# Performance work log

Hardware: AMD Instinct MI355X
Metric: run time of the kernel (lower is better)

## Reference

```python
import jax, jax.numpy as jnp
import numpy as np
from jax import lax

B, S = 32, 128
E, H, V = 300, 1024, 32000


def setup_inputs() -> dict:
    key = jax.random.key(0)
    ks = jax.random.split(key, 6)
    scale = 0.02
    return {
        "sent": jax.random.randint(ks[0], (B, S), 0, V),
        "length": jax.random.randint(ks[1], (B,), 0, S - 1),
        "wordvec": jax.random.normal(ks[2], (V, E), dtype=jnp.float32) * scale,
        "Wxh": jax.random.normal(ks[3], (E, H), dtype=jnp.float32) * scale,
        "Whh": jax.random.normal(ks[4], (H, H), dtype=jnp.float32) * scale,
        "bh": jnp.zeros((H,), dtype=jnp.float32),
        "Wout": jax.random.normal(ks[5], (H, V), dtype=jnp.float32) * scale,
        "bout": jnp.zeros((V,), dtype=jnp.float32),
    }


def reference(sent, length, wordvec, Wxh, Whh, bh, Wout, bout):
    # Embedding lookup for all input positions except the last (teacher forcing)
    emb = wordvec[sent]                      # [B, S, E]
    xs = jnp.swapaxes(emb[:, :-1], 0, 1)     # [S-1, B, E] time-major for scan

    def step(h, x):
        # vanilla RNN cell: h' = tanh(x Wxh + h Whh + b)
        h_new = jnp.tanh(x @ Wxh + h @ Whh + bh)
        return h_new, h_new

    h0 = jnp.zeros((sent.shape[0], Whh.shape[0]), dtype=wordvec.dtype)
    _, hs = lax.scan(step, h0, xs)           # hs: [S-1, B, H]

    # Per-step vocab projection, batched across time in one GEMM
    logits = jnp.einsum('sbh,hv->bsv', hs, Wout) + bout   # [B, S-1, V]

    # Masked cross-entropy against next tokens
    targets = sent[:, 1:]                                  # [B, S-1]
    logp = jax.nn.log_softmax(logits, axis=-1)
    nll = -jnp.take_along_axis(logp, targets[..., None], axis=-1)[..., 0]
    seqlen = sent.shape[1]
    valid = (jnp.arange(seqlen - 1)[None, :] < length[:, None]).astype(logits.dtype)
    loss = (nll * valid).sum() / valid.sum()
    return loss, logits
```

## Files before the change

### kernel.cpp

```cpp
#include <hip/hip_runtime.h>
#include <hip/hip_bf16.h>
#include <stdint.h>

#define B_ 32
#define S_ 128
#define SM1 127
#define E_ 300
#define H_ 1024
#define V_ 32000
#define M_ 4064

typedef __bf16 bf16x8 __attribute__((ext_vector_type(8)));
typedef float f32x4 __attribute__((ext_vector_type(4)));

#define WS_CTR   0
#define WS_NLL   1024
#define WS_HFRAG 4096
#define WS_PRE   135168
#define WS_HS    16781312
#define WS_WBT   25104384

union frag_cvt { f32x4 f; bf16x8 h; };

__device__ __forceinline__ f32x4 coh_load16(const uint8_t* p) {
  f32x4 r;
  asm volatile("global_load_dwordx4 %0, %1, off sc0 sc1"
               : "=v"(r) : "v"(p) : "memory");
  return r;
}
__device__ __forceinline__ void coh_store16(uint8_t* p, f32x4 v) {
  asm volatile("global_store_dwordx4 %0, %1, off sc0 sc1"
               :: "v"(p), "v"(v) : "memory");
}

__global__ __launch_bounds__(256) void k_wout_cvt(const float* __restrict__ Wout,
                                                  __hip_bfloat16* __restrict__ bt) {
  __shared__ float t[32][33];
  int vt = blockIdx.x / 32, kt = blockIdx.x - vt * 32;
  int tx = threadIdx.x & 31, ty = threadIdx.x >> 5;
#pragma unroll
  for (int i = 0; i < 4; i++) {
    int k = kt * 32 + ty + i * 8;
    t[ty + i * 8][tx] = Wout[(size_t)k * V_ + vt * 32 + tx];
  }
  __syncthreads();
#pragma unroll
  for (int i = 0; i < 4; i++) {
    int v = vt * 32 + ty + i * 8;
    bt[(size_t)v * H_ + kt * 32 + tx] = __float2bfloat16(t[tx][ty + i * 8]);
  }
}

__global__ __launch_bounds__(256) void k_pre(const int* __restrict__ sent,
    const float* __restrict__ wordvec, const float* __restrict__ Wxh,
    const float* __restrict__ bh, float* __restrict__ pre) {
  __shared__ float e[8 * E_];
  int r0 = blockIdx.x * 8;
  int s = r0 >> 5, b0 = r0 & 31;
  for (int idx = threadIdx.x; idx < 8 * E_; idx += 256) {
    int i = idx / E_, k = idx - i * E_;
    int tok = sent[(b0 + i) * S_ + s];
    e[idx] = wordvec[(size_t)tok * E_ + k];
  }
  __syncthreads();
  int j0 = threadIdx.x * 4;
  float4 acc[8];
#pragma unroll
  for (int i = 0; i < 8; i++) acc[i] = make_float4(0.f, 0.f, 0.f, 0.f);
  for (int k = 0; k < E_; k++) {
    float4 w = *(const float4*)&Wxh[k * H_ + j0];
#pragma unroll
    for (int i = 0; i < 8; i++) {
      float ev = e[i * E_ + k];
      acc[i].x += ev * w.x; acc[i].y += ev * w.y;
      acc[i].z += ev * w.z; acc[i].w += ev * w.w;
    }
  }
  float4 bias = *(const float4*)&bh[j0];
#pragma unroll
  for (int i = 0; i < 8; i++) {
    float4 o = make_float4(acc[i].x + bias.x, acc[i].y + bias.y,
                           acc[i].z + bias.z, acc[i].w + bias.w);
    *(float4*)&pre[(size_t)(r0 + i) * H_ + j0] = o;
  }
}

__global__ __launch_bounds__(256) void k_rnn(const float* __restrict__ Whh,
    const float* __restrict__ pre, __hip_bfloat16* __restrict__ hs,
    uint8_t* __restrict__ ws) {
  __shared__ __hip_bfloat16 ldsB[32 * 64 * 8];
  __shared__ float ldsP[4 * 8 * 64];
  __shared__ __hip_bfloat16 ldsCt[32 * 24];
  const int jb = blockIdx.x;
  const int tid = threadIdx.x;
  const int lane = tid & 63, w = tid >> 6;
  uint32_t* ctr = (uint32_t*)(ws + WS_CTR);
  uint8_t* hfrag = ws + WS_HFRAG;

  for (int idx = tid; idx < 32 * 64; idx += 256) {
    int kc = idx >> 6, l = idx & 63;
    int n = l & 15;
    int k0 = kc * 32 + ((l >> 4) << 3);
    bf16x8 v;
#pragma unroll
    for (int i = 0; i < 8; i++)
      v[i] = (__bf16)Whh[(size_t)(k0 + i) * H_ + jb * 16 + n];
    *(bf16x8*)&ldsB[idx * 8] = v;
  }
  __syncthreads();

  for (int s = 0; s < SM1; s++) {
    const uint8_t* rbuf = hfrag + ((s & 1) ? 65536 : 0);
    uint8_t* wbuf = hfrag + ((s & 1) ? 0 : 65536);
    f32x4 acc0 = {0.f, 0.f, 0.f, 0.f}, acc1 = {0.f, 0.f, 0.f, 0.f};
    const int kc0 = w * 8;

    bf16x8 a0[8], a1[8];
#pragma unroll
    for (int i = 0; i < 8; i++) {
      int kc = kc0 + i;
      frag_cvt c0, c1;
      c0.f = coh_load16(rbuf + (((kc * 2 + 0) * 64 + lane) << 4));
      c1.f = coh_load16(rbuf + (((kc * 2 + 1) * 64 + lane) << 4));
      a0[i] = c0.h; a1[i] = c1.h;
    }
    asm volatile("s_waitcnt vmcnt(0)" ::: "memory");
    __builtin_amdgcn_sched_barrier(0);
#pragma unroll
    for (int i = 0; i < 8; i++) {
      int kc = kc0 + i;
      bf16x8 b0 = *(const bf16x8*)&ldsB[(kc * 64 + lane) * 8];
      acc0 = __builtin_amdgcn_mfma_f32_16x16x32_bf16(a0[i], b0, acc0, 0, 0, 0);
      acc1 = __builtin_amdgcn_mfma_f32_16x16x32_bf16(a1[i], b0, acc1, 0, 0, 0);
    }
#pragma unroll
    for (int r = 0; r < 4; r++) {
      ldsP[(w * 8 + r) * 64 + lane] = acc0[r];
      ldsP[(w * 8 + 4 + r) * 64 + lane] = acc1[r];
    }
    __syncthreads();
    {
      int t = w >> 1;
      int jl = lane & 15;
#pragma unroll
      for (int rr = 0; rr < 2; rr++) {
        int r = ((w & 1) << 1) + rr;
        float sum = 0.f;
#pragma unroll
        for (int p = 0; p < 4; p++) sum += ldsP[(p * 8 + t * 4 + r) * 64 + lane];
        int b = t * 16 + ((lane >> 4) << 2) + r;
        float x = sum + pre[(size_t)(s * 32 + b) * H_ + jb * 16 + jl];
        float h = tanhf(x);
        __hip_bfloat16 hb = __float2bfloat16(h);
        hs[(size_t)(b * SM1 + s) * H_ + jb * 16 + jl] = hb;
        ldsCt[b * 24 + jl] = hb;
      }
    }
    __syncthreads();
    if (w == 0 && (lane >> 5) == (jb & 1)) {
      int kcw = jb >> 1;
#pragma unroll
      for (int t2 = 0; t2 < 2; t2++) {
        frag_cvt c;
        c.h = *(const bf16x8*)&ldsCt[(t2 * 16 + (lane & 15)) * 24 +
                                     (((lane >> 4) & 1) << 3)];
        coh_store16(wbuf + (((kcw * 2 + t2) * 64 + lane) << 4), c.f);
      }
    }
    if (s < SM1 - 1) {
      if (tid == 0) {
        asm volatile("s_waitcnt vmcnt(0)" ::: "memory");
        __hip_atomic_fetch_add(&ctr[s], 1u, __ATOMIC_RELAXED, __HIP_MEMORY_SCOPE_AGENT);
        while (__hip_atomic_load(&ctr[s], __ATOMIC_RELAXED, __HIP_MEMORY_SCOPE_AGENT) < 64u)
          __builtin_amdgcn_s_sleep(2);
      }
      __syncthreads();
    }
  }
}

__global__ __launch_bounds__(256) void k_gemm(const __hip_bfloat16* __restrict__ A,
    const __hip_bfloat16* __restrict__ Bt, const float* __restrict__ bout,
    float* __restrict__ C) {
  __shared__ __hip_bfloat16 lA[128 * 64];
  __shared__ __hip_bfloat16 lB[128 * 64];
  int bid = blockIdx.x;
  int idx = bid & 255;
  int mt = idx & 31;
  int nt = ((bid >> 8) << 3) + (idx >> 5);
  int tid = threadIdx.x;
  int lane = tid & 63, w = tid >> 6;
  int wm = (w >> 1) << 6, wn = (w & 1) << 6;
  int mbase = mt * 128, nbase = nt * 128;
  f32x4 acc[4][4];
#pragma unroll
  for (int t = 0; t < 4; t++)
#pragma unroll
    for (int u = 0; u < 4; u++) acc[t][u] = (f32x4){0.f, 0.f, 0.f, 0.f};

  for (int k0 = 0; k0 < H_; k0 += 64) {
#pragma unroll
    for (int r = 0; r < 4; r++) {
      int L = r * 4096 + tid * 16;
      int row = L >> 7;
      int gphys = (L >> 4) & 7;
      int glog = gphys ^ (row & 7);
      int m = mbase + row; if (m > M_ - 1) m = M_ - 1;
      const uint8_t* g = (const uint8_t*)A + ((size_t)m * H_ + k0) * 2 + glog * 16;
      __builtin_amdgcn_global_load_lds((const __attribute__((address_space(1))) uint32_t*)g,
          (__attribute__((address_space(3))) uint32_t*)((uint8_t*)lA + L), 16, 0, 0);
    }
#pragma unroll
    for (int r = 0; r < 4; r++) {
      int L = r * 4096 + tid * 16;
      int row = L >> 7;
      int gphys = (L >> 4) & 7;
      int glog = gphys ^ (row & 7);
      int n = nbase + row;
      const uint8_t* g = (const uint8_t*)Bt + ((size_t)n * H_ + k0) * 2 + glog * 16;
      __builtin_amdgcn_global_load_lds((const __attribute__((address_space(1))) uint32_t*)g,
          (__attribute__((address_space(3))) uint32_t*)((uint8_t*)lB + L), 16, 0, 0);
    }
    __builtin_amdgcn_s_waitcnt(0);
    __syncthreads();
#pragma unroll
    for (int kk = 0; kk < 64; kk += 32) {
      bf16x8 af[4], bfr[4];
      int quad = lane >> 4;
#pragma unroll
      for (int t = 0; t < 4; t++) {
        int row = wm + t * 16 + (lane & 15);
        int gphys = ((kk >> 3) + quad) ^ (row & 7);
        af[t] = *(const bf16x8*)&lA[row * 64 + gphys * 8];
      }
#pragma unroll
      for (int u = 0; u < 4; u++) {
        int row = wn + u * 16 + (lane & 15);
        int gphys = ((kk >> 3) + quad) ^ (row & 7);
        bfr[u] = *(const bf16x8*)&lB[row * 64 + gphys * 8];
      }
#pragma unroll
      for (int t = 0; t < 4; t++)
#pragma unroll
        for (int u = 0; u < 4; u++)
          acc[t][u] = __builtin_amdgcn_mfma_f32_16x16x32_bf16(af[t], bfr[u], acc[t][u], 0, 0, 0);
    }
    __syncthreads();
  }
  int quad = lane >> 4, l15 = lane & 15;
#pragma unroll
  for (int u = 0; u < 4; u++) {
    int col = nbase + wn + u * 16 + l15;
    float bias = bout[col];
#pragma unroll
    for (int t = 0; t < 4; t++) {
      int rowb = mbase + wm + t * 16 + quad * 4;
#pragma unroll
      for (int r = 0; r < 4; r++) {
        int row = rowb + r;
        if (row < M_) C[(size_t)row * V_ + col] = acc[t][u][r] + bias;
      }
    }
  }
}

__global__ __launch_bounds__(256) void k_loss(const float* __restrict__ logits,
    const int* __restrict__ sent, const int* __restrict__ length,
    float* __restrict__ nll_acc) {
  int r = blockIdx.x;
  int b = r / SM1, s = r - b * SM1;
  if (s >= length[b]) return;
  const float* row = logits + (size_t)r * V_;
  float m = -3.0e38f, l = 0.f;
  for (int v = threadIdx.x; v < V_; v += 256) {
    float x = row[v];
    float nm = fmaxf(m, x);
    l = l * __expf(m - nm) + __expf(x - nm);
    m = nm;
  }
#pragma unroll
  for (int off = 1; off < 64; off <<= 1) {
    float m2 = __shfl_xor(m, off);
    float l2 = __shfl_xor(l, off);
    float nm = fmaxf(m, m2);
    l = l * __expf(m - nm) + l2 * __expf(m2 - nm);
    m = nm;
  }
  __shared__ float sm[4], sl[4];
  int wv = threadIdx.x >> 6;
  if ((threadIdx.x & 63) == 0) { sm[wv] = m; sl[wv] = l; }
  __syncthreads();
  if (threadIdx.x == 0) {
    m = sm[0]; l = sl[0];
    for (int p = 1; p < 4; p++) {
      float nm = fmaxf(m, sm[p]);
      l = l * __expf(m - nm) + sl[p] * __expf(sm[p] - nm);
      m = nm;
    }
    int tgt = sent[b * S_ + s + 1];
    float nll = m + logf(l) - row[tgt];
    atomicAdd(nll_acc, nll);
  }
}

__global__ void k_final(const float* __restrict__ nll_acc,
                        const int* __restrict__ length, float* __restrict__ out) {
  float cnt = 0.f;
  for (int b = 0; b < B_; b++) cnt += (float)length[b];
  out[0] = nll_acc[0] / cnt;
}

extern "C" void kernel_launch(void* const* d_in, const int* in_sizes, int n_in,
                              void* d_out, int out_size, void* d_ws, size_t ws_size,
                              hipStream_t stream) {
  const int* sent      = (const int*)d_in[0];
  const int* length    = (const int*)d_in[1];
  const float* wordvec = (const float*)d_in[2];
  const float* Wxh     = (const float*)d_in[3];
  const float* Whh     = (const float*)d_in[4];
  const float* bh      = (const float*)d_in[5];
  const float* Wout    = (const float*)d_in[6];
  const float* bout    = (const float*)d_in[7];
  float* out = (float*)d_out;
  uint8_t* ws = (uint8_t*)d_ws;

  hipMemsetAsync(ws, 0, 135168, stream);

  __hip_bfloat16* wbt = (__hip_bfloat16*)(ws + WS_WBT);
  float* pre          = (float*)(ws + WS_PRE);
  __hip_bfloat16* hs  = (__hip_bfloat16*)(ws + WS_HS);
  float* logits       = out + 1;

  k_wout_cvt<<<32000, 256, 0, stream>>>(Wout, wbt);
  k_pre<<<508, 256, 0, stream>>>(sent, wordvec, Wxh, bh, pre);
  k_rnn<<<64, 256, 0, stream>>>(Whh, pre, hs, ws);
  k_gemm<<<8000, 256, 0, stream>>>(hs, wbt, bout, logits);
  k_loss<<<4064, 256, 0, stream>>>(logits, sent, length, (float*)(ws + WS_NLL));
  k_final<<<1, 1, 0, stream>>>((const float*)(ws + WS_NLL), length, out);
}
```

Before: 1.959 ms.

## Double-buffer LDS tiles in vocab GEMM and stage epilogue through LDS

The vocab-projection GEMM now keeps two LDS buffers and issues the global-to-LDS loads for the next K-slice before running MFMAs on the current one, which overlaps memory latency with compute. The epilogue writes accumulators into a padded per-wave LDS tile and then stores rows to global memory as 16-byte vectors instead of scattered scalar stores. In exchange, LDS use grows to about 68 KB per block, which can lower occupancy.

```diff
diff --git a/kernel.cpp b/kernel.cpp
--- a/kernel.cpp
+++ b/kernel.cpp
@@ -182,8 +182,7 @@
 __global__ __launch_bounds__(256) void k_gemm(const __hip_bfloat16* __restrict__ A,
     const __hip_bfloat16* __restrict__ Bt, const float* __restrict__ bout,
     float* __restrict__ C) {
-  __shared__ __hip_bfloat16 lA[128 * 64];
-  __shared__ __hip_bfloat16 lB[128 * 64];
+  __shared__ __align__(16) uint8_t lds[69632];
   int bid = blockIdx.x;
   int idx = bid & 255;
   int mt = idx & 31;
@@ -192,74 +191,92 @@
   int lane = tid & 63, w = tid >> 6;
   int wm = (w >> 1) << 6, wn = (w & 1) << 6;
   int mbase = mt * 128, nbase = nt * 128;
+  int quad = lane >> 4, l15 = lane & 15;
   f32x4 acc[4][4];
 #pragma unroll
   for (int t = 0; t < 4; t++)
 #pragma unroll
     for (int u = 0; u < 4; u++) acc[t][u] = (f32x4){0.f, 0.f, 0.f, 0.f};
 
-  for (int k0 = 0; k0 < H_; k0 += 64) {
+  auto STAGE = [&](int buf, int k0) {
+    uint8_t* dA = lds + buf * 32768;
+    uint8_t* dB = lds + buf * 32768 + 16384;
 #pragma unroll
     for (int r = 0; r < 4; r++) {
       int L = r * 4096 + tid * 16;
       int row = L >> 7;
-      int gphys = (L >> 4) & 7;
-      int glog = gphys ^ (row & 7);
+      int glog = ((L >> 4) & 7) ^ (row & 7);
       int m = mbase + row; if (m > M_ - 1) m = M_ - 1;
       const uint8_t* g = (const uint8_t*)A + ((size_t)m * H_ + k0) * 2 + glog * 16;
       __builtin_amdgcn_global_load_lds((const __attribute__((address_space(1))) uint32_t*)g,
-          (__attribute__((address_space(3))) uint32_t*)((uint8_t*)lA + L), 16, 0, 0);
+          (__attribute__((address_space(3))) uint32_t*)(dA + L), 16, 0, 0);
     }
 #pragma unroll
     for (int r = 0; r < 4; r++) {
       int L = r * 4096 + tid * 16;
       int row = L >> 7;
-      int gphys = (L >> 4) & 7;
-      int glog = gphys ^ (row & 7);
+      int glog = ((L >> 4) & 7) ^ (row & 7);
       int n = nbase + row;
       const uint8_t* g = (const uint8_t*)Bt + ((size_t)n * H_ + k0) * 2 + glog * 16;
       __builtin_amdgcn_global_load_lds((const __attribute__((address_space(1))) uint32_t*)g,
-          (__attribute__((address_space(3))) uint32_t*)((uint8_t*)lB + L), 16, 0, 0);
-    }
-    __builtin_amdgcn_s_waitcnt(0);
-    __syncthreads();
+          (__attribute__((address_space(3))) uint32_t*)(dB + L), 16, 0, 0);
+    }
+  };
+
+  STAGE(0, 0);
+  asm volatile("s_waitcnt vmcnt(0)" ::: "memory");
+  __syncthreads();
+
+  for (int t = 0; t < 16; t++) {
+    int cur = t & 1;
+    if (t < 15) STAGE(cur ^ 1, (t + 1) * 64);
+    const __hip_bfloat16* lA = (const __hip_bfloat16*)(lds + cur * 32768);
+    const __hip_bfloat16* lB = (const __hip_bfloat16*)(lds + cur * 32768 + 16384);
 #pragma unroll
     for (int kk = 0; kk < 64; kk += 32) {
       bf16x8 af[4], bfr[4];
-      int quad = lane >> 4;
-#pragma unroll
-      for (int t = 0; t < 4; t++) {
-        int row = wm + t * 16 + (lane & 15);
+#pragma unroll
+      for (int tt = 0; tt < 4; tt++) {
+        int row = wm + tt * 16 + l15;
         int gphys = ((kk >> 3) + quad) ^ (row & 7);
-        af[t] = *(const bf16x8*)&lA[row * 64 + gphys * 8];
+        af[tt] = *(const bf16x8*)&lA[row * 64 + gphys * 8];
       }
 #pragma unroll
       for (int u = 0; u < 4; u++) {
-        int row = wn + u * 16 + (lane & 15);
+        int row = wn + u * 16 + l15;
         int gphys = ((kk >> 3) + quad) ^ (row & 7);
         bfr[u] = *(const bf16x8*)&lB[row * 64 + gphys * 8];
       }
 #pragma unroll
-      for (int t = 0; t < 4; t++)
+      for (int tt = 0; tt < 4; tt++)
 #pragma unroll
         for (int u = 0; u < 4; u++)
-          acc[t][u] = __builtin_amdgcn_mfma_f32_16x16x32_bf16(af[t], bfr[u], acc[t][u], 0, 0, 0);
-    }
+          acc[tt][u] = __builtin_amdgcn_mfma_f32_16x16x32_bf16(af[tt], bfr[u], acc[tt][u], 0, 0, 0);
+    }
+    asm volatile("s_waitcnt vmcnt(0)" ::: "memory");
     __syncthreads();
   }
-  int quad = lane >> 4, l15 = lane & 15;
+
+  float* ep = (float*)(lds + w * 17408);
 #pragma unroll
   for (int u = 0; u < 4; u++) {
-    int col = nbase + wn + u * 16 + l15;
-    float bias = bout[col];
-#pragma unroll
-    for (int t = 0; t < 4; t++) {
-      int rowb = mbase + wm + t * 16 + quad * 4;
+    float bias = bout[nbase + wn + u * 16 + l15];
+#pragma unroll
+    for (int tt = 0; tt < 4; tt++) {
 #pragma unroll
       for (int r = 0; r < 4; r++) {
-        int row = rowb + r;
-        if (row < M_) C[(size_t)row * V_ + col] = acc[t][u][r] + bias;
-      }
+        int lr = tt * 16 + quad * 4 + r;
+        ep[lr * 68 + u * 16 + l15] = acc[tt][u][r] + bias;
+      }
+    }
+  }
+#pragma unroll
+  for (int i = 0; i < 16; i++) {
+    int lr = i * 4 + quad;
+    int gr = mbase + wm + lr;
+    if (gr < M_) {
+      f32x4 v = *(const f32x4*)&ep[lr * 68 + l15 * 4];
+      *(f32x4*)&C[(size_t)gr * V_ + nbase + wn + l15 * 4] = v;
     }
   }
 }
```

Result: faster. 1.715 ms (-12.5%).
